# Performance work log

Measured on AMD Instinct MI355X. Metric: run time of the kernel, lower is better.

Reference implementation:

```python
import jax, jax.numpy as jnp
import numpy as np

T, N, E, F_IN, H_GNN, H_OUT, RH, G, C = 8, 10000, 160000, 128, 128, 128, 128, 32, 10


def gcn_layer(x, src, dst, W, b):
    # PyG GCNConv: h = D^-1/2 (A+I) D^-1/2 (x W) + b, self-loops added, edge weight 1
    h = x @ W  # [N, H]
    ones = jnp.ones((E,), h.dtype)
    deg = jax.ops.segment_sum(ones, dst, num_segments=N) + 1.0  # +1 for self-loop
    dinv = jax.lax.rsqrt(deg)
    coef = dinv[src] * dinv[dst]  # [E]
    agg = jax.ops.segment_sum(h[src] * coef[:, None], dst, num_segments=N)
    agg = agg + h * (dinv * dinv)[:, None]  # self-loop term
    return agg + b


def snapshot_encode(x, edge_index, batch, W1, b1, W2, b2):
    src, dst = edge_index[0], edge_index[1]
    h = jax.nn.relu(gcn_layer(x, src, dst, W1, b1))
    h = jax.nn.relu(gcn_layer(h, src, dst, W2, b2))
    sums = jax.ops.segment_sum(h, batch, num_segments=G)  # global_mean_pool
    cnts = jax.ops.segment_sum(jnp.ones((N,), h.dtype), batch, num_segments=G)
    return sums / jnp.maximum(cnts, 1.0)[:, None]  # [G, H_OUT]


def gru_layer(seq, Wih, Whh, bih, bhh):
    # seq: [T, G, in]; torch nn.GRU cell equations
    H = Whh.shape[1]

    def step(h, xt):
        gi = xt @ Wih.T + bih
        gh = h @ Whh.T + bhh
        ir, iz, inn = jnp.split(gi, 3, axis=-1)
        hr, hz, hn = jnp.split(gh, 3, axis=-1)
        r = jax.nn.sigmoid(ir + hr)
        z = jax.nn.sigmoid(iz + hz)
        n = jnp.tanh(inn + r * hn)
        h_new = (1.0 - z) * n + z * h
        return h_new, h_new

    h0 = jnp.zeros((seq.shape[1], H), seq.dtype)
    hT, outs = jax.lax.scan(step, h0, seq)
    return outs, hT


def setup_inputs() -> dict:
    key = jax.random.key(0)
    ks = jax.random.split(key, 20)
    s = 0.05
    inp = {
        "x": jax.random.normal(ks[0], (T, N, F_IN), jnp.float32),
        "edge_index": jax.random.randint(ks[1], (T, 2, E), 0, N),
        "batch": jax.random.randint(ks[2], (T, N), 0, G),
        "W1": jax.random.normal(ks[3], (F_IN, H_GNN), jnp.float32) * s,
        "b1": jnp.zeros((H_GNN,), jnp.float32),
        "W2": jax.random.normal(ks[4], (H_GNN, H_OUT), jnp.float32) * s,
        "b2": jnp.zeros((H_OUT,), jnp.float32),
        "Wih0": jax.random.normal(ks[5], (3 * RH, H_OUT), jnp.float32) * s,
        "Whh0": jax.random.normal(ks[6], (3 * RH, RH), jnp.float32) * s,
        "bih0": jnp.zeros((3 * RH,), jnp.float32),
        "bhh0": jnp.zeros((3 * RH,), jnp.float32),
        "Wih1": jax.random.normal(ks[7], (3 * RH, RH), jnp.float32) * s,
        "Whh1": jax.random.normal(ks[8], (3 * RH, RH), jnp.float32) * s,
        "bih1": jnp.zeros((3 * RH,), jnp.float32),
        "bhh1": jnp.zeros((3 * RH,), jnp.float32),
        "Wc": jax.random.normal(ks[9], (C, RH), jnp.float32) * s,
        "bc": jnp.zeros((C,), jnp.float32),
    }
    return inp


def reference(x, edge_index, batch, W1, b1, W2, b2, Wih0, Whh0, bih0, bhh0,
              Wih1, Whh1, bih1, bhh1, Wc, bc):
    # per-snapshot GNN encode, vmapped over T snapshots -> [T, G, H_OUT]
    emb = jax.vmap(snapshot_encode, in_axes=(0, 0, 0, None, None, None, None))(
        x, edge_index, batch, W1, b1, W2, b2)
    outs, _ = gru_layer(emb, Wih0, Whh0, bih0, bhh0)
    _, hT = gru_layer(outs, Wih1, Whh1, bih1, bhh1)  # h_n[-1]: last layer final state
    return hT @ Wc.T + bc  # [G, C]
```

## Files before the change

### kernel.cpp

```cpp
#include <hip/hip_runtime.h>

#define T_ 8
#define N_ 10000
#define E_ 160000
#define G_ 32
#define C_ 10
#define F_ 128

typedef _Float16 f16;
typedef _Float16 f16x2 __attribute__((ext_vector_type(2)));
typedef _Float16 f16x4 __attribute__((ext_vector_type(4)));
typedef _Float16 f16x8 __attribute__((ext_vector_type(8)));
typedef float floatx4 __attribute__((ext_vector_type(4)));

static constexpr size_t ROWS = (size_t)T_ * N_;
static constexpr int NSL = 32;
static constexpr int SLICE = E_ / NSL;

static constexpr size_t OFF_XH    = 0;
static constexpr size_t OFF_A1    = 20480000;
static constexpr size_t OFF_H1    = 40960000;
static constexpr size_t OFF_REC   = 61440000;
static constexpr size_t OFF_CNT   = 66560000;
static constexpr size_t OFF_DINV  = 76800000;
static constexpr size_t OFF_RP    = 77120000;
static constexpr size_t OFF_CNTG  = 77440032;
static constexpr size_t OFF_BRP   = 77441056;
static constexpr size_t OFF_WP    = 77442112;
static constexpr size_t OFF_BLIST = 77507648;
static constexpr size_t OFF_GPACK = 77827648;
static constexpr size_t OFF_PART  = 78220864;

__device__ __forceinline__ float sig_fast(float x) {
  return __builtin_amdgcn_rcpf(1.0f + __builtin_amdgcn_exp2f(-1.4426950408889634f * x));
}
__device__ __forceinline__ float tanh_fast(float x) {
  return 1.0f - 2.0f * __builtin_amdgcn_rcpf(1.0f + __builtin_amdgcn_exp2f(2.8853900817779268f * x));
}

__global__ __launch_bounds__(1024) void prep0_kernel(const int* __restrict__ ei,
                                                     const int* __restrict__ batch,
                                                     int* __restrict__ cnt,
                                                     int* __restrict__ cntG,
                                                     const float* __restrict__ W1,
                                                     const float* __restrict__ W2,
                                                     f16* __restrict__ Wp,
                                                     const float* __restrict__ A0,
                                                     const float* __restrict__ A1,
                                                     const float* __restrict__ A2,
                                                     const float* __restrict__ A3,
                                                     f16* __restrict__ gp) {
  __shared__ int hL[N_];
  __shared__ int cL[G_];
  int b = blockIdx.x, tid = threadIdx.x;
  if (b >= 256) {
    int idx = (b - 256) * 1024 + tid;
    if (idx < 32768) {
      const float* W = (idx < 16384) ? W1 : W2;
      int l = idx & 16383;
      int j = l & 7, lane = (l >> 3) & 63, ct = (l >> 9) & 7, kc = (l >> 12) & 3;
      int k = kc * 32 + ((lane >> 4) & 3) * 8 + j;
      int n = ct * 16 + (lane & 15);
      Wp[idx] = (f16)W[k * 128 + n];
    } else {
      int gidx = idx - 32768;
      int mat = gidx / 49152, l = gidx - mat * 49152;
      int j = l & 7, lane = (l >> 3) & 63, kc = (l >> 9) & 3, nt = l >> 11;
      int k = kc * 32 + ((lane >> 4) & 3) * 8 + j;
      int u = nt * 16 + (lane & 15);
      const float* W = (mat == 0) ? A0 : (mat == 1) ? A1 : (mat == 2) ? A2 : A3;
      gp[gidx] = (f16)W[u * 128 + k];
    }
    return;
  }
  int t = b & 7, s = b >> 3;
  for (int i = tid; i < N_; i += 1024) hL[i] = 0;
  if (tid < G_) cL[tid] = 0;
  __syncthreads();
  const int* dstp = ei + (size_t)t * 2 * E_ + E_ + s * SLICE;
  for (int e4 = tid; e4 < SLICE / 4; e4 += 1024) {
    int4 d = *(const int4*)(dstp + e4 * 4);
    atomicAdd(&hL[d.x], 1); atomicAdd(&hL[d.y], 1);
    atomicAdd(&hL[d.z], 1); atomicAdd(&hL[d.w], 1);
  }
  if (s == 0)
    for (int n = tid; n < N_; n += 1024) atomicAdd(&cL[batch[t * N_ + n]], 1);
  __syncthreads();
  int* cp = cnt + ((size_t)t * NSL + s) * N_;
  for (int i = tid; i < N_; i += 1024) cp[i] = hL[i];
  if (s == 0 && tid < G_) cntG[t * G_ + tid] = cL[tid];
}

__global__ __launch_bounds__(1024) void scan_kernel(int* __restrict__ cnt,
                                                    int* __restrict__ rp,
                                                    float* __restrict__ dinv,
                                                    const int* __restrict__ cntG,
                                                    int* __restrict__ brp) {
  __shared__ int wsum[16];
  __shared__ int carry;
  int t = blockIdx.x, tid = threadIdx.x, lane = tid & 63, wid = tid >> 6;
  if (t == 8) {
    int v = (tid < 256) ? cntG[tid] : 0;
    for (int ofs = 1; ofs < 64; ofs <<= 1) {
      int u = __shfl_up(v, ofs);
      if (lane >= ofs) v += u;
    }
    if (lane == 63 && wid < 4) wsum[wid] = v;
    __syncthreads();
    if (tid < 256) {
      int base = 0;
      for (int w = 0; w < wid; ++w) base += wsum[w];
      if (tid == 0) brp[0] = 0;
      brp[tid + 1] = v + base;
    }
    return;
  }
  if (tid == 0) { carry = 0; rp[t * (N_ + 1)] = 0; }
  __syncthreads();
  for (int c0 = 0; c0 < N_; c0 += 1024) {
    int n = c0 + tid;
    int vs[NSL];
    int deg = 0;
    if (n < N_) {
#pragma unroll
      for (int s = 0; s < NSL; ++s) {
        vs[s] = cnt[((size_t)t * NSL + s) * N_ + n];
        deg += vs[s];
      }
      dinv[t * N_ + n] = rsqrtf((float)deg + 1.0f);
    }
    int v = (n < N_) ? deg : 0;
    int v0 = v;
    for (int ofs = 1; ofs < 64; ofs <<= 1) {
      int u = __shfl_up(v, ofs);
      if (lane >= ofs) v += u;
    }
    if (lane == 63) wsum[wid] = v;
    __syncthreads();
    if (wid == 0) {
      int w = (lane < 16) ? wsum[lane] : 0;
      for (int ofs = 1; ofs < 16; ofs <<= 1) {
        int u = __shfl_up(w, ofs);
        if (lane >= ofs) w += u;
      }
      if (lane < 16) wsum[lane] = w;
    }
    __syncthreads();
    int base = carry + (wid ? wsum[wid - 1] : 0);
    if (n < N_) {
      rp[t * (N_ + 1) + n + 1] = base + v;
      int run = base + v - v0;
#pragma unroll
      for (int s = 0; s < NSL; ++s) {
        int vv = vs[s];
        cnt[((size_t)t * NSL + s) * N_ + n] = run;
        run += vv;
      }
    }
    __syncthreads();
    if (tid == 0) carry += wsum[15];
    __syncthreads();
  }
}

__global__ __launch_bounds__(1024) void cvtfill_kernel(const int* __restrict__ ei,
                                                       const int* __restrict__ base,
                                                       int* __restrict__ rec,
                                                       const int* __restrict__ batch,
                                                       const int* __restrict__ brp,
                                                       int* __restrict__ blist,
                                                       const float* __restrict__ x,
                                                       const float* __restrict__ dinv,
                                                       f16* __restrict__ xh) {
  __shared__ int offL[N_];
  __shared__ int cb[G_];
  int b = blockIdx.x, tid = threadIdx.x;
  if (b >= 256) {
    size_t i = ((size_t)(b - 256) * 1024 + tid) * 4;
    float4 v = *(const float4*)(x + i);
    float d = dinv[i >> 7];
    f16x4 o; o.x = (f16)(v.x * d); o.y = (f16)(v.y * d);
    o.z = (f16)(v.z * d); o.w = (f16)(v.w * d);
    *(f16x4*)(xh + i) = o;
    return;
  }
  int t = b & 7, s = b >> 3;
  const int* bp = base + ((size_t)t * NSL + s) * N_;
  for (int i = tid; i < N_; i += 1024) offL[i] = bp[i];
  if (s == 0 && tid < G_) cb[tid] = brp[t * G_ + tid];
  __syncthreads();
  const int* srcp = ei + (size_t)t * 2 * E_ + s * SLICE;
  const int* dstp = srcp + E_;
  int* rt = rec + (size_t)t * E_;
  for (int e4 = tid; e4 < SLICE / 4; e4 += 1024) {
    int4 sv = *(const int4*)(srcp + e4 * 4);
    int4 dv = *(const int4*)(dstp + e4 * 4);
    int p0 = atomicAdd(&offL[dv.x], 1);
    int p1 = atomicAdd(&offL[dv.y], 1);
    int p2 = atomicAdd(&offL[dv.z], 1);
    int p3 = atomicAdd(&offL[dv.w], 1);
    rt[p0] = sv.x; rt[p1] = sv.y; rt[p2] = sv.z; rt[p3] = sv.w;
  }
  if (s == 0) {
    for (int n = tid; n < N_; n += 1024) {
      int g = batch[t * N_ + n];
      int p = atomicAdd(&cb[g], 1);
      blist[p] = t * N_ + n;
    }
  }
}

__global__ __launch_bounds__(256) void agg_kernel(const f16* __restrict__ X, f16* __restrict__ A,
                                                  const int* __restrict__ rp,
                                                  const int* __restrict__ rec,
                                                  const float* __restrict__ dinv) {
  int wave = threadIdx.x >> 6, lane = threadIdx.x & 63;
  int eg = lane >> 4;
  int cb = (lane & 15) * 8;
  int b = blockIdx.x;
  int t = b & 7, i = b >> 3;
  int n = i * 4 + wave;
  int row = t * N_ + n;
  float ds = dinv[row];
  int beg = rp[t * (N_ + 1) + n], end = rp[t * (N_ + 1) + n + 1];
  beg = __builtin_amdgcn_readfirstlane(beg);
  end = __builtin_amdgcn_readfirstlane(end);
  const int* rcb = rec + (size_t)t * E_ + beg + eg;
  const f16* Xt = X + (size_t)t * N_ * F_;

  float s[8] = {0.f, 0.f, 0.f, 0.f, 0.f, 0.f, 0.f, 0.f};
  if (eg == 3) {
    f16x8 v = *(const f16x8*)(Xt + (size_t)n * F_ + cb);
#pragma unroll
    for (int j = 0; j < 8; ++j) s[j] += (float)v[j];
  }
  int cnt = end - beg;
  int nq = cnt >> 2;
  if (nq > 0) {
    int ridA = rcb[0];
    int ridB = (nq > 1) ? rcb[4] : 0;
    int ridC = (nq > 2) ? rcb[8] : 0;
    f16x8 vA = *(const f16x8*)(Xt + (size_t)ridA * F_ + cb);
    f16x8 vB;
    if (nq > 1) vB = *(const f16x8*)(Xt + (size_t)ridB * F_ + cb);
    for (int q = 0; q + 2 < nq; ++q) {
      f16x8 vC = *(const f16x8*)(Xt + (size_t)ridC * F_ + cb);
      int ridD = rcb[(q + 3) * 4];
#pragma unroll
      for (int j = 0; j < 8; ++j) s[j] += (float)vA[j];
      vA = vB; vB = vC; ridC = ridD;
    }
#pragma unroll
    for (int j = 0; j < 8; ++j) s[j] += (float)vA[j];
    if (nq > 1) {
#pragma unroll
      for (int j = 0; j < 8; ++j) s[j] += (float)vB[j];
    }
  }
  int rem = cnt & 3;
  if (eg < rem) {
    int rid = rcb[nq * 4];
    f16x8 v = *(const f16x8*)(Xt + (size_t)rid * F_ + cb);
#pragma unroll
    for (int j = 0; j < 8; ++j) s[j] += (float)v[j];
  }
#pragma unroll
  for (int j = 0; j < 8; ++j) {
    s[j] += __shfl_xor(s[j], 16);
    s[j] += __shfl_xor(s[j], 32);
  }
  if (eg == 0) {
    f16x8 o;
#pragma unroll
    for (int j = 0; j < 8; ++j) o[j] = (f16)(ds * s[j]);
    *(f16x8*)(A + (size_t)row * F_ + cb) = o;
  }
}

__global__ __launch_bounds__(256) void gemm_kernel(const f16* __restrict__ A,
                                                   const f16* __restrict__ Wp,
                                                   const float* __restrict__ bias,
                                                   const float* __restrict__ scale,
                                                   f16* __restrict__ O) {
  __shared__ f16x8 Bp[2048];
  const f16x8* Wv = (const f16x8*)Wp;
  for (int i = threadIdx.x; i < 2048; i += 256) Bp[i] = Wv[i];
  __syncthreads();
  int wave = threadIdx.x >> 6, lane = threadIdx.x & 63;
  int quad = lane >> 4, m = lane & 15;
  int rowbase = blockIdx.x * 64 + wave * 16;
  const f16x8* Arow = (const f16x8*)(A + (size_t)(rowbase + m) * F_);
  floatx4 acc[8];
#pragma unroll
  for (int ct = 0; ct < 8; ++ct) { floatx4 z = {0.f, 0.f, 0.f, 0.f}; acc[ct] = z; }
#pragma unroll
  for (int kc = 0; kc < 4; ++kc) {
    f16x8 a = Arow[kc * 4 + quad];
#pragma unroll
    for (int ct = 0; ct < 8; ++ct)
      acc[ct] = __builtin_amdgcn_mfma_f32_16x16x32_f16(a, Bp[(kc * 8 + ct) * 64 + lane],
                                                       acc[ct], 0, 0, 0);
  }
  float sv[4];
#pragma unroll
  for (int r = 0; r < 4; ++r)
    sv[r] = scale ? scale[rowbase + quad * 4 + r] : 1.0f;
#pragma unroll
  for (int ct = 0; ct < 8; ++ct) {
    int colc = ct * 16 + m;
    float bv = bias[colc];
#pragma unroll
    for (int r = 0; r < 4; ++r) {
      int row = rowbase + quad * 4 + r;
      float v = fmaxf(acc[ct][r] + bv, 0.0f) * sv[r];
      O[(size_t)row * F_ + colc] = (f16)v;
    }
  }
}

__global__ void pool1_kernel(const f16* __restrict__ H, const int* __restrict__ brp,
                             const int* __restrict__ blist, float* __restrict__ part) {
  int b = blockIdx.x;
  int wave = threadIdx.x >> 6, lane = threadIdx.x & 63;
  int idx = b >> 1;
  int s = (b & 1) * 4 + wave;
  int beg = brp[idx], end = brp[idx + 1];
  beg = __builtin_amdgcn_readfirstlane(beg);
  end = __builtin_amdgcn_readfirstlane(end);
  int len = end - beg;
  int lo = beg + (int)(((long long)len * s) >> 3);
  int hi = beg + (int)(((long long)len * (s + 1)) >> 3);
  float a00 = 0.f, a01 = 0.f, a10 = 0.f, a11 = 0.f;
  float a20 = 0.f, a21 = 0.f, a30 = 0.f, a31 = 0.f;
  int e = lo;
  for (; e + 3 < hi; e += 4) {
    int r0 = blist[e], r1 = blist[e + 1], r2 = blist[e + 2], r3 = blist[e + 3];
    f16x2 v0 = *(const f16x2*)(H + (size_t)r0 * F_ + 2 * lane);
    f16x2 v1 = *(const f16x2*)(H + (size_t)r1 * F_ + 2 * lane);
    f16x2 v2 = *(const f16x2*)(H + (size_t)r2 * F_ + 2 * lane);
    f16x2 v3 = *(const f16x2*)(H + (size_t)r3 * F_ + 2 * lane);
    a00 += (float)v0.x; a01 += (float)v0.y;
    a10 += (float)v1.x; a11 += (float)v1.y;
    a20 += (float)v2.x; a21 += (float)v2.y;
    a30 += (float)v3.x; a31 += (float)v3.y;
  }
  for (; e < hi; ++e) {
    int r = blist[e];
    f16x2 v = *(const f16x2*)(H + (size_t)r * F_ + 2 * lane);
    a00 += (float)v.x; a01 += (float)v.y;
  }
  float2 o;
  o.x = (a00 + a10) + (a20 + a30);
  o.y = (a01 + a11) + (a21 + a31);
  *(float2*)(part + ((size_t)idx * 8 + s) * F_ + 2 * lane) = o;
}

__global__ __launch_bounds__(256, 1) void gru_mega(
    const f16* __restrict__ gp, const float* __restrict__ part,
    const int* __restrict__ brp,
    const float* __restrict__ bih0, const float* __restrict__ bhh0,
    const float* __restrict__ bih1, const float* __restrict__ bhh1,
    const float* __restrict__ Wc, const float* __restrict__ bc,
    float* __restrict__ out) {
  __shared__ f16 emb_l[16][136];
  __shared__ float gib0[16][384];
  __shared__ f16 hb0[16 * 136];
  __shared__ f16 hb1[16 * 136];
  __shared__ float ghb[2 * 384];
  __shared__ float gib[2 * 384];
  __shared__ float h1s[2 * 128];
  int tid = threadIdx.x, wave = tid >> 6, lane = tid & 63;
  int quad = lane >> 4, mm = lane & 15;
  int g2 = tid >> 7, f = tid & 127;
  int bid = blockIdx.x;

  {
    int r = tid >> 4;
    int fb = (tid & 15) * 8;
    int idx = (r >> 1) * G_ + bid * 2 + (r & 1);
    float s[8] = {0.f, 0.f, 0.f, 0.f, 0.f, 0.f, 0.f, 0.f};
#pragma unroll
    for (int k = 0; k < 8; ++k) {
      const float* p = part + ((size_t)idx * 8 + k) * F_ + fb;
      float4 v0 = *(const float4*)p;
      float4 v1 = *(const float4*)(p + 4);
      s[0] += v0.x; s[1] += v0.y; s[2] += v0.z; s[3] += v0.w;
      s[4] += v1.x; s[5] += v1.y; s[6] += v1.z; s[7] += v1.w;
    }
    float d = fmaxf((float)(brp[idx + 1] - brp[idx]), 1.0f);
    f16x8 ev;
#pragma unroll
    for (int j = 0; j < 8; ++j) ev[j] = (f16)(s[j] / d);
    *(f16x8*)(&emb_l[r][fb]) = ev;
  }
  __syncthreads();

  {
    floatx4 acc[6];
#pragma unroll
    for (int i = 0; i < 6; ++i) { floatx4 z = {0.f, 0.f, 0.f, 0.f}; acc[i] = z; }
#pragma unroll
    for (int kc = 0; kc < 4; ++kc) {
      f16x8 a = *(const f16x8*)(&emb_l[mm][kc * 32 + quad * 8]);
#pragma unroll
      for (int i = 0; i < 6; ++i) {
        int nt = wave * 6 + i;
        f16x8 bf = *(const f16x8*)(gp + (size_t)((nt * 4 + kc) * 64 + lane) * 8);
        acc[i] = __builtin_amdgcn_mfma_f32_16x16x32_f16(a, bf, acc[i], 0, 0, 0);
      }
    }
#pragma unroll
    for (int i = 0; i < 6; ++i)
#pragma unroll
      for (int r = 0; r < 4; ++r)
        gib0[quad * 4 + r][(wave * 6 + i) * 16 + mm] = acc[i][r];
  }

  f16x8 B0[24], B1[24];
#pragma unroll
  for (int i = 0; i < 6; ++i)
#pragma unroll
    for (int kc = 0; kc < 4; ++kc) {
      size_t off = (size_t)((((wave * 6 + i) * 4 + kc) * 64 + lane)) * 8;
      B0[i * 4 + kc] = *(const f16x8*)(gp + 1 * 49152 + off);
      B1[i * 4 + kc] = *(const f16x8*)(gp + 3 * 49152 + off);
    }
  float br0 = bih0[f] + bhh0[f];
  float bz0 = bih0[128 + f] + bhh0[128 + f];
  float bni0 = bih0[256 + f], bnh0 = bhh0[256 + f];
  float br1 = bih1[f] + bhh1[f];
  float bz1 = bih1[128 + f] + bhh1[128 + f];
  float bni1 = bih1[256 + f], bnh1 = bhh1[256 + f];

  for (int i = tid; i < 16 * 136; i += 256) { hb0[i] = (f16)0.f; hb1[i] = (f16)0.f; }
  float h0 = 0.f, h1 = 0.f;
  __syncthreads();

  const f16* wih1 = gp + 2 * 49152;
  for (int t = 0; t < T_; ++t) {
    f16x8 Bs[24];
#pragma unroll
    for (int i = 0; i < 6; ++i)
#pragma unroll
      for (int kc = 0; kc < 4; ++kc)
        Bs[i * 4 + kc] = *(const f16x8*)(wih1 +
            (size_t)((((wave * 6 + i) * 4 + kc) * 64 + lane)) * 8);
    const float* gi = &gib0[t * 2 + g2][0];
    float gir = gi[f], giz = gi[128 + f], gin = gi[256 + f];

    floatx4 acc[6];
#pragma unroll
    for (int i = 0; i < 6; ++i) { floatx4 z = {0.f, 0.f, 0.f, 0.f}; acc[i] = z; }
#pragma unroll
    for (int kc = 0; kc < 4; ++kc) {
      f16x8 a = *(const f16x8*)(hb0 + mm * 136 + kc * 32 + quad * 8);
#pragma unroll
      for (int i = 0; i < 6; ++i)
        acc[i] = __builtin_amdgcn_mfma_f32_16x16x32_f16(a, B0[i * 4 + kc], acc[i], 0, 0, 0);
    }
    if (quad == 0) {
#pragma unroll
      for (int i = 0; i < 6; ++i) {
        ghb[0 * 384 + wave * 96 + i * 16 + mm] = acc[i][0];
        ghb[1 * 384 + wave * 96 + i * 16 + mm] = acc[i][1];
      }
    }
    __syncthreads();

    {
      float hr = ghb[g2 * 384 + f];
      float hz = ghb[g2 * 384 + 128 + f];
      float hn = ghb[g2 * 384 + 256 + f];
      float r = sig_fast(gir + hr + br0);
      float z = sig_fast(giz + hz + bz0);
      float nn = tanh_fast(gin + bni0 + r * (hn + bnh0));
      h0 = (1.0f - z) * nn + z * h0;
      hb0[g2 * 136 + f] = (f16)h0;
    }
    __syncthreads();

    floatx4 accx[6], acch[6];
#pragma unroll
    for (int i = 0; i < 6; ++i) {
      floatx4 z = {0.f, 0.f, 0.f, 0.f}; accx[i] = z; acch[i] = z;
    }
#pragma unroll
    for (int kc = 0; kc < 4; ++kc) {
      f16x8 ax = *(const f16x8*)(hb0 + mm * 136 + kc * 32 + quad * 8);
      f16x8 ah = *(const f16x8*)(hb1 + mm * 136 + kc * 32 + quad * 8);
#pragma unroll
      for (int i = 0; i < 6; ++i) {
        accx[i] = __builtin_amdgcn_mfma_f32_16x16x32_f16(ax, Bs[i * 4 + kc], accx[i], 0, 0, 0);
        acch[i] = __builtin_amdgcn_mfma_f32_16x16x32_f16(ah, B1[i * 4 + kc], acch[i], 0, 0, 0);
      }
    }
    if (quad == 0) {
#pragma unroll
      for (int i = 0; i < 6; ++i) {
        gib[0 * 384 + wave * 96 + i * 16 + mm] = accx[i][0];
        gib[1 * 384 + wave * 96 + i * 16 + mm] = accx[i][1];
        ghb[0 * 384 + wave * 96 + i * 16 + mm] = acch[i][0];
        ghb[1 * 384 + wave * 96 + i * 16 + mm] = acch[i][1];
      }
    }
    __syncthreads();

    {
      float i1r = gib[g2 * 384 + f];
      float i1z = gib[g2 * 384 + 128 + f];
      float i1n = gib[g2 * 384 + 256 + f];
      float hr = ghb[g2 * 384 + f];
      float hz = ghb[g2 * 384 + 128 + f];
      float hn = ghb[g2 * 384 + 256 + f];
      float r = sig_fast(i1r + hr + br1);
      float z = sig_fast(i1z + hz + bz1);
      float nn = tanh_fast(i1n + bni1 + r * (hn + bnh1));
      h1 = (1.0f - z) * nn + z * h1;
      hb1[g2 * 136 + f] = (f16)h1;
    }
    __syncthreads();
  }

  h1s[g2 * 128 + f] = h1;
  __syncthreads();
  if (tid < 2 * C_) {
    int gg = tid / C_, c = tid - gg * C_;
    float s = bc[c];
    const float* wr = Wc + (size_t)c * 128;
    const float* hr = h1s + gg * 128;
    for (int k = 0; k < 128; k += 4) {
      float4 w = *(const float4*)(wr + k);
      s += hr[k] * w.x + hr[k + 1] * w.y + hr[k + 2] * w.z + hr[k + 3] * w.w;
    }
    out[(bid * 2 + gg) * C_ + c] = s;
  }
}

extern "C" void kernel_launch(void* const* d_in, const int* in_sizes, int n_in,
                              void* d_out, int out_size, void* d_ws, size_t ws_size,
                              hipStream_t stream) {
  const float* x    = (const float*)d_in[0];
  const int*   ei   = (const int*)d_in[1];
  const int*   batch= (const int*)d_in[2];
  const float* W1   = (const float*)d_in[3];
  const float* b1   = (const float*)d_in[4];
  const float* W2   = (const float*)d_in[5];
  const float* b2   = (const float*)d_in[6];
  const float* Wih0 = (const float*)d_in[7];
  const float* Whh0 = (const float*)d_in[8];
  const float* bih0 = (const float*)d_in[9];
  const float* bhh0 = (const float*)d_in[10];
  const float* Wih1 = (const float*)d_in[11];
  const float* Whh1 = (const float*)d_in[12];
  const float* bih1 = (const float*)d_in[13];
  const float* bhh1 = (const float*)d_in[14];
  const float* Wc   = (const float*)d_in[15];
  const float* bc   = (const float*)d_in[16];
  float* out = (float*)d_out;

  char* ws = (char*)d_ws;
  f16*   Xh    = (f16*)(ws + OFF_XH);
  f16*   A1    = (f16*)(ws + OFF_A1);
  f16*   H1    = (f16*)(ws + OFF_H1);
  f16*   A2    = A1;
  f16*   H2    = Xh;
  int*   rec   = (int*)(ws + OFF_REC);
  int*   cnt   = (int*)(ws + OFF_CNT);
  float* dinv  = (float*)(ws + OFF_DINV);
  int*   rp    = (int*)(ws + OFF_RP);
  int*   cntG  = (int*)(ws + OFF_CNTG);
  int*   brp   = (int*)(ws + OFF_BRP);
  f16*   Wp    = (f16*)(ws + OFF_WP);
  int*   blist = (int*)(ws + OFF_BLIST);
  f16*   gp    = (f16*)(ws + OFF_GPACK);
  float* part  = (float*)(ws + OFF_PART);

  prep0_kernel<<<480, 1024, 0, stream>>>(ei, batch, cnt, cntG,
                                         W1, W2, Wp, Wih0, Whh0, Wih1, Whh1, gp);
  scan_kernel<<<9, 1024, 0, stream>>>(cnt, rp, dinv, cntG, brp);
  cvtfill_kernel<<<2756, 1024, 0, stream>>>(ei, cnt, rec, batch, brp, blist, x, dinv, Xh);

  agg_kernel<<<20000, 256, 0, stream>>>(Xh, A1, rp, rec, dinv);
  gemm_kernel<<<1250, 256, 0, stream>>>(A1, Wp, b1, dinv, H1);
  agg_kernel<<<20000, 256, 0, stream>>>(H1, A2, rp, rec, dinv);
  gemm_kernel<<<1250, 256, 0, stream>>>(A2, Wp + 16384, b2, (const float*)nullptr, H2);

  pool1_kernel<<<512, 256, 0, stream>>>(H2, brp, blist, part);
  gru_mega<<<16, 256, 0, stream>>>(gp, part, brp, bih0, bhh0, bih1, bhh1, Wc, bc, out);
}
```

Baseline: 295.1 us.

## Replace sliced LDS histograms with global-atomic degree counting and CSR fill

Degree counting and the CSR fill move from 32 per-slice LDS histograms (10000-entry shared arrays, 1024-thread blocks) to direct global atomics on a single per-snapshot degree and offset array. This drops the 32-way partial count buffers, their write-out and the 32-way summation in the scan, and lets small 256-thread blocks run with high occupancy. A separate zero/pack kernel clears the counters, so there is one extra launch. Global atomics contend more than LDS atomics, and the edge order within each CSR row becomes nondeterministic.

```diff
diff --git a/kernel.cpp b/kernel.cpp
--- a/kernel.cpp
+++ b/kernel.cpp
@@ -13,15 +13,13 @@
 typedef _Float16 f16x8 __attribute__((ext_vector_type(8)));
 typedef float floatx4 __attribute__((ext_vector_type(4)));
 
-static constexpr size_t ROWS = (size_t)T_ * N_;
-static constexpr int NSL = 32;
-static constexpr int SLICE = E_ / NSL;
-
 static constexpr size_t OFF_XH    = 0;
 static constexpr size_t OFF_A1    = 20480000;
 static constexpr size_t OFF_H1    = 40960000;
 static constexpr size_t OFF_REC   = 61440000;
-static constexpr size_t OFF_CNT   = 66560000;
+static constexpr size_t OFF_DEG   = 66560000;
+static constexpr size_t OFF_OFS   = 66880000;
+static constexpr size_t OFF_CBG   = 67200000;
 static constexpr size_t OFF_DINV  = 76800000;
 static constexpr size_t OFF_RP    = 77120000;
 static constexpr size_t OFF_CNTG  = 77440032;
@@ -38,72 +36,85 @@
   return 1.0f - 2.0f * __builtin_amdgcn_rcpf(1.0f + __builtin_amdgcn_exp2f(2.8853900817779268f * x));
 }
 
-__global__ __launch_bounds__(1024) void prep0_kernel(const int* __restrict__ ei,
-                                                     const int* __restrict__ batch,
-                                                     int* __restrict__ cnt,
-                                                     int* __restrict__ cntG,
-                                                     const float* __restrict__ W1,
-                                                     const float* __restrict__ W2,
-                                                     f16* __restrict__ Wp,
-                                                     const float* __restrict__ A0,
-                                                     const float* __restrict__ A1,
-                                                     const float* __restrict__ A2,
-                                                     const float* __restrict__ A3,
-                                                     f16* __restrict__ gp) {
-  __shared__ int hL[N_];
-  __shared__ int cL[G_];
+__global__ __launch_bounds__(256) void zero_pack_kernel(const float* __restrict__ W1,
+                                                        const float* __restrict__ W2,
+                                                        f16* __restrict__ Wp,
+                                                        const float* __restrict__ A0,
+                                                        const float* __restrict__ A1,
+                                                        const float* __restrict__ A2,
+                                                        const float* __restrict__ A3,
+                                                        f16* __restrict__ gp,
+                                                        int4* __restrict__ deg4,
+                                                        int4* __restrict__ cntG4) {
+  int idx = blockIdx.x * 256 + threadIdx.x;
+  int4 z4 = {0, 0, 0, 0};
+  if (idx < 20000) deg4[idx] = z4;
+  if (idx < 64) cntG4[idx] = z4;
+  if (idx < 32768) {
+    const float* W = (idx < 16384) ? W1 : W2;
+    int l = idx & 16383;
+    int j = l & 7, lane = (l >> 3) & 63, ct = (l >> 9) & 7, kc = (l >> 12) & 3;
+    int k = kc * 32 + ((lane >> 4) & 3) * 8 + j;
+    int n = ct * 16 + (lane & 15);
+    Wp[idx] = (f16)W[k * 128 + n];
+  } else if (idx < 229376) {
+    int gidx = idx - 32768;
+    int mat = gidx / 49152, l = gidx - mat * 49152;
+    int j = l & 7, lane = (l >> 3) & 63, kc = (l >> 9) & 3, nt = l >> 11;
+    int k = kc * 32 + ((lane >> 4) & 3) * 8 + j;
+    int u = nt * 16 + (lane & 15);
+    const float* W = (mat == 0) ? A0 : (mat == 1) ? A1 : (mat == 2) ? A2 : A3;
+    gp[gidx] = (f16)W[u * 128 + k];
+  }
+}
+
+__global__ __launch_bounds__(256) void hist_kernel(const int* __restrict__ ei,
+                                                   const int* __restrict__ batch,
+                                                   int* __restrict__ deg,
+                                                   int* __restrict__ cntG) {
+  __shared__ int cL[256];
   int b = blockIdx.x, tid = threadIdx.x;
-  if (b >= 256) {
-    int idx = (b - 256) * 1024 + tid;
-    if (idx < 32768) {
-      const float* W = (idx < 16384) ? W1 : W2;
-      int l = idx & 16383;
-      int j = l & 7, lane = (l >> 3) & 63, ct = (l >> 9) & 7, kc = (l >> 12) & 3;
-      int k = kc * 32 + ((lane >> 4) & 3) * 8 + j;
-      int n = ct * 16 + (lane & 15);
-      Wp[idx] = (f16)W[k * 128 + n];
-    } else {
-      int gidx = idx - 32768;
-      int mat = gidx / 49152, l = gidx - mat * 49152;
-      int j = l & 7, lane = (l >> 3) & 63, kc = (l >> 9) & 3, nt = l >> 11;
-      int k = kc * 32 + ((lane >> 4) & 3) * 8 + j;
-      int u = nt * 16 + (lane & 15);
-      const float* W = (mat == 0) ? A0 : (mat == 1) ? A1 : (mat == 2) ? A2 : A3;
-      gp[gidx] = (f16)W[u * 128 + k];
-    }
+  if (b < 1250) {
+    int i4 = b * 256 + tid;
+    int elem = i4 * 4;
+    int t = elem / E_;
+    int e = elem - t * E_;
+    const int4 d = *(const int4*)(ei + (size_t)t * 2 * E_ + E_ + e);
+    int* dt = deg + t * N_;
+    atomicAdd(&dt[d.x], 1); atomicAdd(&dt[d.y], 1);
+    atomicAdd(&dt[d.z], 1); atomicAdd(&dt[d.w], 1);
     return;
   }
-  int t = b & 7, s = b >> 3;
-  for (int i = tid; i < N_; i += 1024) hL[i] = 0;
-  if (tid < G_) cL[tid] = 0;
-  __syncthreads();
-  const int* dstp = ei + (size_t)t * 2 * E_ + E_ + s * SLICE;
-  for (int e4 = tid; e4 < SLICE / 4; e4 += 1024) {
-    int4 d = *(const int4*)(dstp + e4 * 4);
-    atomicAdd(&hL[d.x], 1); atomicAdd(&hL[d.y], 1);
-    atomicAdd(&hL[d.z], 1); atomicAdd(&hL[d.w], 1);
-  }
-  if (s == 0)
-    for (int n = tid; n < N_; n += 1024) atomicAdd(&cL[batch[t * N_ + n]], 1);
-  __syncthreads();
-  int* cp = cnt + ((size_t)t * NSL + s) * N_;
-  for (int i = tid; i < N_; i += 1024) cp[i] = hL[i];
-  if (s == 0 && tid < G_) cntG[t * G_ + tid] = cL[tid];
-}
-
-__global__ __launch_bounds__(1024) void scan_kernel(int* __restrict__ cnt,
+  cL[tid] = 0;
+  __syncthreads();
+  int i4 = (b - 1250) * 256 + tid;
+  if (i4 < 20000) {
+    int flat = i4 * 4;
+    int t = flat / N_;
+    int4 g = *(const int4*)(batch + flat);
+    atomicAdd(&cL[t * G_ + g.x], 1); atomicAdd(&cL[t * G_ + g.y], 1);
+    atomicAdd(&cL[t * G_ + g.z], 1); atomicAdd(&cL[t * G_ + g.w], 1);
+  }
+  __syncthreads();
+  if (cL[tid]) atomicAdd(&cntG[tid], cL[tid]);
+}
+
+__global__ __launch_bounds__(1024) void scan_kernel(const int* __restrict__ deg,
                                                     int* __restrict__ rp,
+                                                    int* __restrict__ ofs,
                                                     float* __restrict__ dinv,
                                                     const int* __restrict__ cntG,
-                                                    int* __restrict__ brp) {
+                                                    int* __restrict__ brp,
+                                                    int* __restrict__ cbg) {
   __shared__ int wsum[16];
   __shared__ int carry;
   int t = blockIdx.x, tid = threadIdx.x, lane = tid & 63, wid = tid >> 6;
   if (t == 8) {
-    int v = (tid < 256) ? cntG[tid] : 0;
-    for (int ofs = 1; ofs < 64; ofs <<= 1) {
-      int u = __shfl_up(v, ofs);
-      if (lane >= ofs) v += u;
+    int c = (tid < 256) ? cntG[tid] : 0;
+    int v = c;
+    for (int ofs_ = 1; ofs_ < 64; ofs_ <<= 1) {
+      int u = __shfl_up(v, ofs_);
+      if (lane >= ofs_) v += u;
     }
     if (lane == 63 && wid < 4) wsum[wid] = v;
     __syncthreads();
@@ -112,6 +123,7 @@
       for (int w = 0; w < wid; ++w) base += wsum[w];
       if (tid == 0) brp[0] = 0;
       brp[tid + 1] = v + base;
+      cbg[tid] = v + base - c;
     }
     return;
   }
@@ -119,29 +131,23 @@
   __syncthreads();
   for (int c0 = 0; c0 < N_; c0 += 1024) {
     int n = c0 + tid;
-    int vs[NSL];
-    int deg = 0;
+    int dg = 0;
     if (n < N_) {
-#pragma unroll
-      for (int s = 0; s < NSL; ++s) {
-        vs[s] = cnt[((size_t)t * NSL + s) * N_ + n];
-        deg += vs[s];
-      }
-      dinv[t * N_ + n] = rsqrtf((float)deg + 1.0f);
-    }
-    int v = (n < N_) ? deg : 0;
-    int v0 = v;
-    for (int ofs = 1; ofs < 64; ofs <<= 1) {
-      int u = __shfl_up(v, ofs);
-      if (lane >= ofs) v += u;
+      dg = deg[t * N_ + n];
+      dinv[t * N_ + n] = rsqrtf((float)dg + 1.0f);
+    }
+    int v = dg;
+    for (int ofs_ = 1; ofs_ < 64; ofs_ <<= 1) {
+      int u = __shfl_up(v, ofs_);
+      if (lane >= ofs_) v += u;
     }
     if (lane == 63) wsum[wid] = v;
     __syncthreads();
     if (wid == 0) {
       int w = (lane < 16) ? wsum[lane] : 0;
-      for (int ofs = 1; ofs < 16; ofs <<= 1) {
-        int u = __shfl_up(w, ofs);
-        if (lane >= ofs) w += u;
+      for (int ofs_ = 1; ofs_ < 16; ofs_ <<= 1) {
+        int u = __shfl_up(w, ofs_);
+        if (lane >= ofs_) w += u;
       }
       if (lane < 16) wsum[lane] = w;
     }
@@ -149,13 +155,7 @@
     int base = carry + (wid ? wsum[wid - 1] : 0);
     if (n < N_) {
       rp[t * (N_ + 1) + n + 1] = base + v;
-      int run = base + v - v0;
-#pragma unroll
-      for (int s = 0; s < NSL; ++s) {
-        int vv = vs[s];
-        cnt[((size_t)t * NSL + s) * N_ + n] = run;
-        run += vv;
-      }
+      ofs[t * N_ + n] = base + v - dg;
     }
     __syncthreads();
     if (tid == 0) carry += wsum[15];
@@ -163,20 +163,35 @@
   }
 }
 
-__global__ __launch_bounds__(1024) void cvtfill_kernel(const int* __restrict__ ei,
-                                                       const int* __restrict__ base,
-                                                       int* __restrict__ rec,
-                                                       const int* __restrict__ batch,
-                                                       const int* __restrict__ brp,
-                                                       int* __restrict__ blist,
-                                                       const float* __restrict__ x,
-                                                       const float* __restrict__ dinv,
-                                                       f16* __restrict__ xh) {
-  __shared__ int offL[N_];
-  __shared__ int cb[G_];
+__global__ __launch_bounds__(256) void cvtfill_kernel(const int* __restrict__ ei,
+                                                      int* __restrict__ ofs,
+                                                      int* __restrict__ rec,
+                                                      const int* __restrict__ batch,
+                                                      int* __restrict__ cbg,
+                                                      int* __restrict__ blist,
+                                                      const float* __restrict__ x,
+                                                      const float* __restrict__ dinv,
+                                                      f16* __restrict__ xh) {
   int b = blockIdx.x, tid = threadIdx.x;
-  if (b >= 256) {
-    size_t i = ((size_t)(b - 256) * 1024 + tid) * 4;
+  if (b < 1250) {
+    int i4 = b * 256 + tid;
+    int elem = i4 * 4;
+    int t = elem / E_;
+    int e = elem - t * E_;
+    const int* srcp = ei + (size_t)t * 2 * E_ + e;
+    int4 sv = *(const int4*)srcp;
+    int4 dv = *(const int4*)(srcp + E_);
+    int* ot = ofs + t * N_;
+    int* rt = rec + (size_t)t * E_;
+    int p0 = atomicAdd(&ot[dv.x], 1);
+    int p1 = atomicAdd(&ot[dv.y], 1);
+    int p2 = atomicAdd(&ot[dv.z], 1);
+    int p3 = atomicAdd(&ot[dv.w], 1);
+    rt[p0] = sv.x; rt[p1] = sv.y; rt[p2] = sv.z; rt[p3] = sv.w;
+    return;
+  }
+  if (b < 11250) {
+    size_t i = ((size_t)(b - 1250) * 256 + tid) * 4;
     float4 v = *(const float4*)(x + i);
     float d = dinv[i >> 7];
     f16x4 o; o.x = (f16)(v.x * d); o.y = (f16)(v.y * d);
@@ -184,29 +199,12 @@
     *(f16x4*)(xh + i) = o;
     return;
   }
-  int t = b & 7, s = b >> 3;
-  const int* bp = base + ((size_t)t * NSL + s) * N_;
-  for (int i = tid; i < N_; i += 1024) offL[i] = bp[i];
-  if (s == 0 && tid < G_) cb[tid] = brp[t * G_ + tid];
-  __syncthreads();
-  const int* srcp = ei + (size_t)t * 2 * E_ + s * SLICE;
-  const int* dstp = srcp + E_;
-  int* rt = rec + (size_t)t * E_;
-  for (int e4 = tid; e4 < SLICE / 4; e4 += 1024) {
-    int4 sv = *(const int4*)(srcp + e4 * 4);
-    int4 dv = *(const int4*)(dstp + e4 * 4);
-    int p0 = atomicAdd(&offL[dv.x], 1);
-    int p1 = atomicAdd(&offL[dv.y], 1);
-    int p2 = atomicAdd(&offL[dv.z], 1);
-    int p3 = atomicAdd(&offL[dv.w], 1);
-    rt[p0] = sv.x; rt[p1] = sv.y; rt[p2] = sv.z; rt[p3] = sv.w;
-  }
-  if (s == 0) {
-    for (int n = tid; n < N_; n += 1024) {
-      int g = batch[t * N_ + n];
-      int p = atomicAdd(&cb[g], 1);
-      blist[p] = t * N_ + n;
-    }
+  int idx = (b - 11250) * 256 + tid;
+  if (idx < 80000) {
+    int t = idx / N_;
+    int g = batch[idx];
+    int p = atomicAdd(&cbg[t * G_ + g], 1);
+    blist[p] = idx;
   }
 }
 
@@ -565,7 +563,9 @@
   f16*   A2    = A1;
   f16*   H2    = Xh;
   int*   rec   = (int*)(ws + OFF_REC);
-  int*   cnt   = (int*)(ws + OFF_CNT);
+  int*   deg   = (int*)(ws + OFF_DEG);
+  int*   ofs   = (int*)(ws + OFF_OFS);
+  int*   cbg   = (int*)(ws + OFF_CBG);
   float* dinv  = (float*)(ws + OFF_DINV);
   int*   rp    = (int*)(ws + OFF_RP);
   int*   cntG  = (int*)(ws + OFF_CNTG);
@@ -575,10 +575,11 @@
   f16*   gp    = (f16*)(ws + OFF_GPACK);
   float* part  = (float*)(ws + OFF_PART);
 
-  prep0_kernel<<<480, 1024, 0, stream>>>(ei, batch, cnt, cntG,
-                                         W1, W2, Wp, Wih0, Whh0, Wih1, Whh1, gp);
-  scan_kernel<<<9, 1024, 0, stream>>>(cnt, rp, dinv, cntG, brp);
-  cvtfill_kernel<<<2756, 1024, 0, stream>>>(ei, cnt, rec, batch, brp, blist, x, dinv, Xh);
+  zero_pack_kernel<<<1024, 256, 0, stream>>>(W1, W2, Wp, Wih0, Whh0, Wih1, Whh1, gp,
+                                             (int4*)deg, (int4*)cntG);
+  hist_kernel<<<1329, 256, 0, stream>>>(ei, batch, deg, cntG);
+  scan_kernel<<<9, 1024, 0, stream>>>(deg, rp, ofs, dinv, cntG, brp, cbg);
+  cvtfill_kernel<<<11563, 256, 0, stream>>>(ei, ofs, rec, batch, cbg, blist, x, dinv, Xh);
 
   agg_kernel<<<20000, 256, 0, stream>>>(Xh, A1, rp, rec, dinv);
   gemm_kernel<<<1250, 256, 0, stream>>>(A1, Wp, b1, dinv, H1);
```

Result: slower. 398.6 us (+35.1%).
